# Kernel optimization log

Hardware: AMD Instinct MI355X
Metric: run time of the kernel (lower is better)

Reference implementation:

```python
import jax, jax.numpy as jnp
import numpy as np

N_NODES = 50000

def setup_inputs() -> dict:
    key = jax.random.key(0)
    k1, k2, k3, k4, k5 = jax.random.split(key, 5)
    x = jax.random.normal(k1, (50000, 128), dtype=jnp.float32)
    weight = jax.random.normal(k2, (128, 32), dtype=jnp.float32) * (np.sqrt(6.0 / (128 + 32)))
    edge_src = jax.random.randint(k3, (1600000,), 0, N_NODES, dtype=jnp.int32)
    edge_dst = jax.random.randint(k4, (1600000,), 0, N_NODES, dtype=jnp.int32)
    edge_weight = jax.random.uniform(k5, (1600000,), dtype=jnp.float32)
    return {"x": x, "weight": weight, "edge_src": edge_src,
            "edge_dst": edge_dst, "edge_weight": edge_weight}

def reference(x, weight, edge_src, edge_dst, edge_weight):
    # h = x @ W  (dense GEMM)
    h = x @ weight                                   # [N, out]
    # out = spmm(adj, h): gather h rows at src, scale by edge weight,
    # scatter-add into dst rows (COO SpMM).
    msgs = edge_weight[:, None] * h[edge_src]        # [E, out]
    out = jax.ops.segment_sum(msgs, edge_dst, num_segments=N_NODES)
    return out
```

## Files before the change

kernel.cpp:

```cpp
#include <hip/hip_runtime.h>
#include <hip/hip_bf16.h>
#include <stdint.h>

#define N_NODES   50000
#define K_DIM     128
#define OUT_DIM   32
#define N_EDGES   1600000
#define NBKT      782
#define CAP       3072
#define AFIT      16
#define FB        ((N_EDGES + 256*AFIT - 1) / (256*AFIT))
#define GB        ((N_NODES + 63) / 64)
#define XSTR      136

typedef __attribute__((ext_vector_type(8))) short bf16x8;
typedef __attribute__((ext_vector_type(4))) float f32x4;

__global__ __launch_bounds__(256) void zero_cursor(int* __restrict__ cursor) {
    for (int i = threadIdx.x; i < NBKT; i += 256) cursor[i] = 0;
}

__global__ __launch_bounds__(256) void gemm_fill(const float* __restrict__ x,
                                                 const float* __restrict__ w,
                                                 __hip_bfloat16* __restrict__ h,
                                                 const int*   __restrict__ esrc,
                                                 const int*   __restrict__ edst,
                                                 const float* __restrict__ ew,
                                                 int*         __restrict__ cursor,
                                                 uint64_t*    __restrict__ pairs) {
    __shared__ __align__(16) char smem[40192];
    const int t = threadIdx.x;

    if (blockIdx.x < FB) {
        int*      cnt   = (int*)smem;
        int*      wbase = (int*)(smem + 3200);
        int*      scr   = (int*)(smem + 6400);
        uint64_t* stg   = (uint64_t*)(smem + 7424);

        for (int i = t; i < 800; i += 256) cnt[i] = 0;
        __syncthreads();

        uint32_t lo[AFIT], hi[AFIT];
        uint16_t rk[AFIT];
        const int base = blockIdx.x * 256 * AFIT;
        #pragma unroll
        for (int k = 0; k < AFIT; ++k) {
            const int e = base + k * 256 + t;
            if (e < N_EDGES) {
                const uint32_t s = (uint32_t)esrc[e];
                const uint32_t d = (uint32_t)edst[e];
                lo[k] = (d << 16) | s;
                hi[k] = __float_as_uint(ew[e]);
                rk[k] = (uint16_t)atomicAdd(&cnt[d >> 6], 1);
            } else {
                lo[k] = 0xffffffffu;
            }
        }
        __syncthreads();
        for (int i = t; i < NBKT; i += 256) {
            const int c = cnt[i];
            if (c) wbase[i] = atomicAdd(&cursor[i], c);
        }
        __syncthreads();
        int v0[4]; int lsum = 0;
        #pragma unroll
        for (int j = 0; j < 4; ++j) { v0[j] = (t * 4 + j < 800) ? cnt[t * 4 + j] : 0; lsum += v0[j]; }
        scr[t] = lsum;
        __syncthreads();
        #pragma unroll
        for (int d = 1; d < 256; d <<= 1) {
            const int a = (t >= d) ? scr[t - d] : 0;
            __syncthreads();
            scr[t] += a;
            __syncthreads();
        }
        int run = scr[t] - lsum;
        #pragma unroll
        for (int j = 0; j < 4; ++j) {
            if (t * 4 + j < 800) { const int c = v0[j]; cnt[t * 4 + j] = run; run += c; }
        }
        __syncthreads();
        #pragma unroll
        for (int k = 0; k < AFIT; ++k) {
            if (lo[k] != 0xffffffffu) {
                const int b = (int)(lo[k] >> 22);
                stg[cnt[b] + (int)rk[k]] = ((uint64_t)hi[k] << 32) | lo[k];
            }
        }
        __syncthreads();
        const int total = min(256 * AFIT, N_EDGES - base);
        for (int i = t; i < total; i += 256) {
            const uint64_t p = stg[i];
            const int b    = (int)((p >> 22) & 0x3ff);
            const int gpos = wbase[b] + i - cnt[b];
            if (gpos < CAP)
                pairs[(size_t)b * CAP + gpos] = p;
        }
    } else {
        uint16_t* wt = (uint16_t*)smem;
        uint16_t* xt = (uint16_t*)(smem + 8704);

        for (int i = t; i < K_DIM * OUT_DIM; i += 256) {
            const int k = i >> 5, c = i & 31;
            const __hip_bfloat16 bv = __float2bfloat16(w[i]);
            wt[c * XSTR + k] = *(const uint16_t*)&bv;
        }
        const int row0 = (blockIdx.x - FB) * 64;
        const float4* xg4 = reinterpret_cast<const float4*>(x);
        const long long gmax4 = (long long)N_NODES * (K_DIM / 4);
        #pragma unroll
        for (int i = 0; i < 8; ++i) {
            const int idx = i * 256 + t;
            const int row = idx >> 5;
            const int k4  = idx & 31;
            const long long gi = (long long)(row0 + row) * (K_DIM / 4) + k4;
            float4 v = make_float4(0.f, 0.f, 0.f, 0.f);
            if (gi < gmax4) v = xg4[gi];
            __hip_bfloat16 b0 = __float2bfloat16(v.x), b1 = __float2bfloat16(v.y);
            __hip_bfloat16 b2 = __float2bfloat16(v.z), b3 = __float2bfloat16(v.w);
            ushort4 u;
            u.x = *(const uint16_t*)&b0; u.y = *(const uint16_t*)&b1;
            u.z = *(const uint16_t*)&b2; u.w = *(const uint16_t*)&b3;
            *reinterpret_cast<ushort4*>(xt + row * XSTR + k4 * 4) = u;
        }
        __syncthreads();

        const int wv   = t >> 6;
        const int lane = t & 63;
        const int m    = lane & 15;
        const int kg   = lane >> 4;

        f32x4 acc0 = {0.f, 0.f, 0.f, 0.f};
        f32x4 acc1 = {0.f, 0.f, 0.f, 0.f};
        const uint16_t* arow = xt + (wv * 16 + m) * XSTR;
        const uint16_t* b0p  = wt + m * XSTR;
        const uint16_t* b1p  = wt + (16 + m) * XSTR;
        #pragma unroll
        for (int s = 0; s < 4; ++s) {
            const int k0 = s * 32 + kg * 8;
            const bf16x8 a  = *reinterpret_cast<const bf16x8*>(arow + k0);
            const bf16x8 b0 = *reinterpret_cast<const bf16x8*>(b0p + k0);
            const bf16x8 b1 = *reinterpret_cast<const bf16x8*>(b1p + k0);
            acc0 = __builtin_amdgcn_mfma_f32_16x16x32_bf16(a, b0, acc0, 0, 0, 0);
            acc1 = __builtin_amdgcn_mfma_f32_16x16x32_bf16(a, b1, acc1, 0, 0, 0);
        }
        #pragma unroll
        for (int r = 0; r < 4; ++r) {
            const int grow = row0 + wv * 16 + kg * 4 + r;
            if (grow < N_NODES) {
                h[(size_t)grow * OUT_DIM + m]      = __float2bfloat16(acc0[r]);
                h[(size_t)grow * OUT_DIM + 16 + m] = __float2bfloat16(acc1[r]);
            }
        }
    }
}

__global__ __launch_bounds__(512) void sort_pull(const int*      __restrict__ cursor,
                                                 const uint64_t* __restrict__ pairs,
                                                 const __hip_bfloat16* __restrict__ h,
                                                 float*          __restrict__ out) {
    __shared__ uint64_t stg[CAP];
    __shared__ int lcnt[64];
    __shared__ int loff[65];
    const int b    = blockIdx.x;
    const int t    = threadIdx.x;
    const size_t beg = (size_t)b * CAP;
    const int cnt  = min(cursor[b], CAP);
    const int wv   = t >> 6;
    const int lane = t & 63;
    const int col  = lane & 31;
    const int half = lane >> 5;

    if (t < 64) lcnt[t] = 0;
    __syncthreads();

    uint64_t pl[6];
    int      pr[6];
    #pragma unroll
    for (int k = 0; k < 6; ++k) {
        const int i = t + k * 512;
        if (i < cnt) {
            const uint64_t p = pairs[beg + i];
            const int nl = (int)((p >> 16) & 63);
            pl[k] = p;
            pr[k] = (nl << 12) | atomicAdd(&lcnt[nl], 1);
        } else {
            pr[k] = -1;
        }
    }
    __syncthreads();
    if (t < 64) {
        const int v = lcnt[t];
        int p = v;
        #pragma unroll
        for (int d = 1; d < 64; d <<= 1) {
            const int n = __shfl_up(p, d, 64);
            if (t >= d) p += n;
        }
        loff[t] = p - v;
        if (t == 63) loff[64] = p;
    }
    __syncthreads();
    #pragma unroll
    for (int k = 0; k < 6; ++k) {
        if (pr[k] >= 0)
            stg[loff[pr[k] >> 12] + (pr[k] & 0xfff)] = pl[k];
    }
    __syncthreads();

    for (int nl = wv * 8; nl < wv * 8 + 8; ++nl) {
        const int node = (b << 6) + nl;
        if (node >= N_NODES) break;
        const int jb = loff[nl], je = loff[nl + 1];
        float acc = 0.f;
        int j = jb + half;
        for (; j + 6 < je; j += 8) {
            const uint64_t p0 = stg[j];
            const uint64_t p1 = stg[j + 2];
            const uint64_t p2 = stg[j + 4];
            const uint64_t p3 = stg[j + 6];
            const float a0 = __bfloat162float(h[(size_t)(p0 & 0xffffu) * OUT_DIM + col]);
            const float a1 = __bfloat162float(h[(size_t)(p1 & 0xffffu) * OUT_DIM + col]);
            const float a2 = __bfloat162float(h[(size_t)(p2 & 0xffffu) * OUT_DIM + col]);
            const float a3 = __bfloat162float(h[(size_t)(p3 & 0xffffu) * OUT_DIM + col]);
            acc += __uint_as_float((uint32_t)(p0 >> 32)) * a0;
            acc += __uint_as_float((uint32_t)(p1 >> 32)) * a1;
            acc += __uint_as_float((uint32_t)(p2 >> 32)) * a2;
            acc += __uint_as_float((uint32_t)(p3 >> 32)) * a3;
        }
        for (; j < je; j += 2) {
            const uint64_t p = stg[j];
            acc += __uint_as_float((uint32_t)(p >> 32)) *
                   __bfloat162float(h[(size_t)(p & 0xffffu) * OUT_DIM + col]);
        }
        acc += __shfl_xor(acc, 32, 64);
        if (half == 0) out[(size_t)node * OUT_DIM + col] = acc;
    }
}

__global__ __launch_bounds__(256) void gemm_only(const float* __restrict__ x,
                                                 const float* __restrict__ w,
                                                 __hip_bfloat16* __restrict__ h) {
    __shared__ float wlds[K_DIM * OUT_DIM];
    const int t = threadIdx.x;
    #pragma unroll
    for (int i = 0; i < (K_DIM * OUT_DIM) / 256; ++i)
        wlds[i * 256 + t] = w[i * 256 + t];
    __syncthreads();
    const int row = blockIdx.x * 8 + (t >> 5);
    const int col = t & 31;
    if (row >= N_NODES) return;
    const float4* x4 = reinterpret_cast<const float4*>(x + (size_t)row * K_DIM);
    float acc = 0.f;
    #pragma unroll
    for (int k4 = 0; k4 < K_DIM / 4; ++k4) {
        float4 xv = x4[k4];
        const int k = k4 * 4;
        acc += xv.x * wlds[(k + 0) * OUT_DIM + col] + xv.y * wlds[(k + 1) * OUT_DIM + col]
             + xv.z * wlds[(k + 2) * OUT_DIM + col] + xv.w * wlds[(k + 3) * OUT_DIM + col];
    }
    h[(size_t)row * OUT_DIM + col] = __float2bfloat16(acc);
}

__global__ __launch_bounds__(256) void scatter_kernel(const int*   __restrict__ esrc,
                                                      const int*   __restrict__ edst,
                                                      const float* __restrict__ ew,
                                                      const __hip_bfloat16* __restrict__ h,
                                                      float*       out) {
    const long long gid = (long long)blockIdx.x * blockDim.x + threadIdx.x;
    const int e   = (int)(gid >> 5);
    const int col = (int)(gid & 31);
    if (e >= N_EDGES) return;
    atomicAdd(out + (size_t)edst[e] * OUT_DIM + col,
              ew[e] * __bfloat162float(h[(size_t)esrc[e] * OUT_DIM + col]));
}

extern "C" void kernel_launch(void* const* d_in, const int* in_sizes, int n_in,
                              void* d_out, int out_size, void* d_ws, size_t ws_size,
                              hipStream_t stream) {
    const float* x    = (const float*)d_in[0];
    const float* w    = (const float*)d_in[1];
    const int*   esrc = (const int*)d_in[2];
    const int*   edst = (const int*)d_in[3];
    const float* ew   = (const float*)d_in[4];
    float*       out  = (float*)d_out;

    const size_t PAIRS_B = (size_t)NBKT * CAP * 8;
    const size_t H_B     = (size_t)N_NODES * OUT_DIM * 2;
    const size_t CUR_B   = (size_t)NBKT * 4;
    const size_t REQ     = PAIRS_B + H_B + CUR_B;

    uint64_t*        pairs  = (uint64_t*)d_ws;
    __hip_bfloat16*  h      = (__hip_bfloat16*)((char*)d_ws + PAIRS_B);
    int*             cursor = (int*)((char*)d_ws + PAIRS_B + H_B);

    if (ws_size >= REQ) {
        zero_cursor<<<1, 256, 0, stream>>>(cursor);
        gemm_fill<<<FB + GB, 256, 0, stream>>>(x, w, h, esrc, edst, ew, cursor, pairs);
        sort_pull<<<NBKT, 512, 0, stream>>>(cursor, pairs, h, out);
    } else {
        __hip_bfloat16* hf = (__hip_bfloat16*)d_ws;
        (void)hipMemsetAsync(d_out, 0, (size_t)out_size * sizeof(float), stream);
        gemm_only<<<(N_NODES + 7) / 8, 256, 0, stream>>>(x, w, hf);
        const long long total = (long long)N_EDGES * OUT_DIM;
        scatter_kernel<<<(int)((total + 255) / 256), 256, 0, stream>>>(esrc, edst, ew, hf, out);
    }
}
```

Measured before the change: 56.12 us.

## Vectorize SpMM pull gather: 8 lanes per row, 8 edges per wave concurrently

The per-node aggregation loop changes from 32 lanes each loading one bf16 column (two edges per wave) to 8 lanes each loading four bf16 values as a 64-bit word, so eight edges are processed concurrently per wave. Each lane keeps four fp32 accumulators and unpacks bf16 with shifts and masks. Partial sums are reduced with three xor-shuffle stages and written as float4. The aim is fewer, wider gather loads and more edge-level parallelism per node, at the cost of extra shuffle reduction and more idle lanes on low-degree nodes.

```diff
diff --git a/kernel.cpp b/kernel.cpp
--- a/kernel.cpp
+++ b/kernel.cpp
@@ -168,8 +168,8 @@
     const int cnt  = min(cursor[b], CAP);
     const int wv   = t >> 6;
     const int lane = t & 63;
-    const int col  = lane & 31;
-    const int half = lane >> 5;
+    const int cq   = lane & 7;
+    const int sl   = lane >> 3;
 
     if (t < 64) lcnt[t] = 0;
     __syncthreads();
@@ -208,33 +208,48 @@
     }
     __syncthreads();
 
+    const uint2* h64 = reinterpret_cast<const uint2*>(h);
     for (int nl = wv * 8; nl < wv * 8 + 8; ++nl) {
         const int node = (b << 6) + nl;
         if (node >= N_NODES) break;
         const int jb = loff[nl], je = loff[nl + 1];
-        float acc = 0.f;
-        int j = jb + half;
-        for (; j + 6 < je; j += 8) {
+        float a0 = 0.f, a1 = 0.f, a2 = 0.f, a3 = 0.f;
+        int j = jb + sl;
+        for (; j + 8 < je; j += 16) {
             const uint64_t p0 = stg[j];
-            const uint64_t p1 = stg[j + 2];
-            const uint64_t p2 = stg[j + 4];
-            const uint64_t p3 = stg[j + 6];
-            const float a0 = __bfloat162float(h[(size_t)(p0 & 0xffffu) * OUT_DIM + col]);
-            const float a1 = __bfloat162float(h[(size_t)(p1 & 0xffffu) * OUT_DIM + col]);
-            const float a2 = __bfloat162float(h[(size_t)(p2 & 0xffffu) * OUT_DIM + col]);
-            const float a3 = __bfloat162float(h[(size_t)(p3 & 0xffffu) * OUT_DIM + col]);
-            acc += __uint_as_float((uint32_t)(p0 >> 32)) * a0;
-            acc += __uint_as_float((uint32_t)(p1 >> 32)) * a1;
-            acc += __uint_as_float((uint32_t)(p2 >> 32)) * a2;
-            acc += __uint_as_float((uint32_t)(p3 >> 32)) * a3;
-        }
-        for (; j < je; j += 2) {
+            const uint64_t p1 = stg[j + 8];
+            const uint2 v0 = h64[(size_t)(p0 & 0xffffu) * 8 + cq];
+            const uint2 v1 = h64[(size_t)(p1 & 0xffffu) * 8 + cq];
+            const float w0 = __uint_as_float((uint32_t)(p0 >> 32));
+            const float w1 = __uint_as_float((uint32_t)(p1 >> 32));
+            a0 += w0 * __uint_as_float(v0.x << 16);
+            a1 += w0 * __uint_as_float(v0.x & 0xffff0000u);
+            a2 += w0 * __uint_as_float(v0.y << 16);
+            a3 += w0 * __uint_as_float(v0.y & 0xffff0000u);
+            a0 += w1 * __uint_as_float(v1.x << 16);
+            a1 += w1 * __uint_as_float(v1.x & 0xffff0000u);
+            a2 += w1 * __uint_as_float(v1.y << 16);
+            a3 += w1 * __uint_as_float(v1.y & 0xffff0000u);
+        }
+        if (j < je) {
             const uint64_t p = stg[j];
-            acc += __uint_as_float((uint32_t)(p >> 32)) *
-                   __bfloat162float(h[(size_t)(p & 0xffffu) * OUT_DIM + col]);
-        }
-        acc += __shfl_xor(acc, 32, 64);
-        if (half == 0) out[(size_t)node * OUT_DIM + col] = acc;
+            const uint2 v = h64[(size_t)(p & 0xffffu) * 8 + cq];
+            const float w = __uint_as_float((uint32_t)(p >> 32));
+            a0 += w * __uint_as_float(v.x << 16);
+            a1 += w * __uint_as_float(v.x & 0xffff0000u);
+            a2 += w * __uint_as_float(v.y << 16);
+            a3 += w * __uint_as_float(v.y & 0xffff0000u);
+        }
+        a0 += __shfl_xor(a0, 8, 64);  a1 += __shfl_xor(a1, 8, 64);
+        a2 += __shfl_xor(a2, 8, 64);  a3 += __shfl_xor(a3, 8, 64);
+        a0 += __shfl_xor(a0, 16, 64); a1 += __shfl_xor(a1, 16, 64);
+        a2 += __shfl_xor(a2, 16, 64); a3 += __shfl_xor(a3, 16, 64);
+        a0 += __shfl_xor(a0, 32, 64); a1 += __shfl_xor(a1, 32, 64);
+        a2 += __shfl_xor(a2, 32, 64); a3 += __shfl_xor(a3, 32, 64);
+        if (sl == 0) {
+            float4* o4 = reinterpret_cast<float4*>(out + (size_t)node * OUT_DIM);
+            o4[cq] = make_float4(a0, a1, a2, a3);
+        }
     }
 }
 
```

After: 53.29 us. 1.05x faster.
